# Kernel tuning notes

Measured on AMD Instinct MI355X. Metric: run time of the kernel, lower is better.

Reference implementation:

```python
import jax, jax.numpy as jnp
import numpy as np

D_MODEL = 1024
N_HEADS = 16
HEAD_DIM = D_MODEL // N_HEADS


def setup_inputs() -> dict:
    key = jax.random.key(0)
    k1, k2, k3 = jax.random.split(key, 3)
    x = jax.random.normal(k1, (4, 2048, D_MODEL), dtype=jnp.float32)
    # torch nn.Linear(d_model, 3*d_model, bias=False): weight [3C, C], y = x @ W.T
    w_qkv = jax.random.normal(k2, (3 * D_MODEL, D_MODEL), dtype=jnp.float32) * (1.0 / np.sqrt(D_MODEL))
    w_out = jax.random.normal(k3, (D_MODEL, D_MODEL), dtype=jnp.float32) * (1.0 / np.sqrt(D_MODEL))
    return {"x": x, "w_qkv": w_qkv, "w_out": w_out}


def reference(x, w_qkv, w_out):
    B, T, C = x.shape
    H, Dh = N_HEADS, HEAD_DIM
    scale = 1.0 / np.sqrt(Dh).astype(np.float32)
    qkv = x @ w_qkv.T  # [B, T, 3C]
    q, k, v = jnp.split(qkv, 3, axis=-1)

    def heads(t):  # [B,T,C] -> [B,H,T,Dh]
        return t.reshape(B, T, H, Dh).transpose(0, 2, 1, 3)

    q, k, v = heads(q), heads(k), heads(v)
    attn = jnp.einsum('bhqd,bhkd->bhqk', q, k) * scale  # [B,H,T,T]
    attn = jax.nn.softmax(attn, axis=-1)
    out = jnp.einsum('bhqk,bhkd->bhqd', attn, v)  # [B,H,T,Dh]
    out = out.transpose(0, 2, 1, 3).reshape(B, T, C)
    return out @ w_out.T
```

## Files before the change

kernel.cpp:

```cpp
#include <hip/hip_runtime.h>
#include <hip/hip_bf16.h>

#define DEVINL __device__ __forceinline__

typedef short s16x8 __attribute__((ext_vector_type(8)));
typedef float f32x4 __attribute__((ext_vector_type(4)));

static constexpr int TC = 1024;
static constexpr int NH = 16;
static constexpr int DH = 64;
static constexpr int TT = 2048;
static constexpr int NB = 4;
static constexpr int MROWS = NB * TT;

static constexpr float QSCALE = 0.18033688011112042f;

DEVINL ushort f32_to_bf16u(float f) {
  uint u = __builtin_bit_cast(uint, f);
  u += 0x7fffu + ((u >> 16) & 1u);
  return (ushort)(u >> 16);
}

DEVINL f32x4 mfma32(s16x8 a, s16x8 b, f32x4 c) {
  return __builtin_amdgcn_mfma_f32_16x16x32_bf16(a, b, c, 0, 0, 0);
}

DEVINL void gload_lds16(const void* g, void* l) {
  __builtin_amdgcn_global_load_lds((const __attribute__((address_space(1))) void*)g,
                                   (__attribute__((address_space(3))) void*)l, 16, 0, 0);
}

DEVINL s16x8 ld8(const ushort* p) { return *reinterpret_cast<const s16x8*>(p); }

DEVINL void cvt_range(const float* __restrict__ src, ushort* __restrict__ dst, int n4,
                      int i0, int stride) {
  for (int i = i0; i < n4; i += stride) {
    float4 v = reinterpret_cast<const float4*>(src)[i];
    ushort4 o;
    o.x = f32_to_bf16u(v.x);
    o.y = f32_to_bf16u(v.y);
    o.z = f32_to_bf16u(v.z);
    o.w = f32_to_bf16u(v.w);
    reinterpret_cast<ushort4*>(dst)[i] = o;
  }
}

__global__ void cvt3_kernel(const float* __restrict__ s0, ushort* __restrict__ d0, int n0,
                            const float* __restrict__ s1, ushort* __restrict__ d1, int n1,
                            const float* __restrict__ s2, ushort* __restrict__ d2, int n2) {
  const int i0 = blockIdx.x * blockDim.x + threadIdx.x;
  const int stride = gridDim.x * blockDim.x;
  cvt_range(s0, d0, n0, i0, stride);
  cvt_range(s1, d1, n1, i0, stride);
  cvt_range(s2, d2, n2, i0, stride);
}

template <int MODE>
__global__ __launch_bounds__(256, 2) void gemm_bt(
    const ushort* __restrict__ A, const ushort* __restrict__ Bw, float* __restrict__ Cout,
    ushort* __restrict__ Qo, ushort* __restrict__ Ko, ushort* __restrict__ Vo, int N) {
  __shared__ __align__(16) ushort As[128 * 128];
  __shared__ __align__(16) ushort Bs[128 * 128];
  const int tid = threadIdx.x;
  const int lane = tid & 63;
  const int wid = tid >> 6;
  const int bx = blockIdx.x, by = blockIdx.y;
  const int wrow = (wid >> 1) * 64, wcol = (wid & 1) * 64;

  f32x4 acc[4][4] = {};

  for (int kt = 0; kt < TC; kt += 128) {
#pragma unroll
    for (int j = 0; j < 8; ++j) {
      const int flat = j * 256 + tid;
      const int r = flat >> 4, ch = flat & 15;
      const int sc = ch ^ (r & 15);
      gload_lds16(A + (size_t)(by * 128 + r) * TC + kt + sc * 8, &As[flat * 8]);
      gload_lds16(Bw + (size_t)(bx * 128 + r) * TC + kt + sc * 8, &Bs[flat * 8]);
    }
    __syncthreads();
#pragma unroll
    for (int kk = 0; kk < 4; ++kk) {
      s16x8 af[4], bfr[4];
#pragma unroll
      for (int m = 0; m < 4; ++m) {
        const int r = wrow + m * 16 + (lane & 15);
        const int ch = (kk * 4 + (lane >> 4)) ^ (r & 15);
        af[m] = ld8(&As[r * 128 + ch * 8]);
      }
#pragma unroll
      for (int n = 0; n < 4; ++n) {
        const int r = wcol + n * 16 + (lane & 15);
        const int ch = (kk * 4 + (lane >> 4)) ^ (r & 15);
        bfr[n] = ld8(&Bs[r * 128 + ch * 8]);
      }
#pragma unroll
      for (int m = 0; m < 4; ++m)
#pragma unroll
        for (int n = 0; n < 4; ++n) acc[m][n] = mfma32(af[m], bfr[n], acc[m][n]);
    }
    __syncthreads();
  }

#pragma unroll
  for (int m = 0; m < 4; ++m) {
#pragma unroll
    for (int n = 0; n < 4; ++n) {
      const int ng = bx * 128 + wcol + n * 16 + (lane & 15);
      const int mg0 = by * 128 + wrow + m * 16 + (lane >> 4) * 4;
      if (MODE == 0) {
#pragma unroll
        for (int i = 0; i < 4; ++i) Cout[(size_t)(mg0 + i) * N + ng] = acc[m][n][i];
      } else {
        const int sec = ng >> 10;
        const int w = ng & 1023;
        const int h = w >> 6, d = w & 63;
        const int t0 = mg0 & (TT - 1);
        const int b = mg0 >> 11;
        const int bh = b * NH + h;
        if (sec == 0) {
#pragma unroll
          for (int i = 0; i < 4; ++i)
            Qo[((size_t)bh * TT + t0 + i) * DH + d] = f32_to_bf16u(acc[m][n][i] * QSCALE);
        } else if (sec == 1) {
#pragma unroll
          for (int i = 0; i < 4; ++i)
            Ko[((size_t)bh * TT + t0 + i) * DH + d] = f32_to_bf16u(acc[m][n][i]);
        } else {
          ushort4 o;
          o.x = f32_to_bf16u(acc[m][n][0]);
          o.y = f32_to_bf16u(acc[m][n][1]);
          o.z = f32_to_bf16u(acc[m][n][2]);
          o.w = f32_to_bf16u(acc[m][n][3]);
          *reinterpret_cast<ushort4*>(&Vo[((size_t)bh * DH + d) * TT + t0]) = o;
        }
      }
    }
  }
}

__global__ __launch_bounds__(256, 4) void attn_kernel(const ushort* __restrict__ Q,
                                                      const ushort* __restrict__ K,
                                                      const ushort* __restrict__ V,
                                                      ushort* __restrict__ O) {
  __shared__ __align__(16) ushort Ks[2][64 * 64];
  __shared__ __align__(16) ushort Vs[2][64 * 64];
  const int tid = threadIdx.x;
  const int lane = tid & 63, wid = tid >> 6;
  const int bh = blockIdx.x;
  const int q0 = blockIdx.y * 128 + wid * 32;
  const int qr = lane & 15, lg = lane >> 4;

  const ushort* Qh = Q + (size_t)bh * TT * DH;
  const ushort* Kh = K + (size_t)bh * TT * DH;
  const ushort* Vh = V + (size_t)bh * DH * TT;

  s16x8 qf[2][2];
#pragma unroll
  for (int qt = 0; qt < 2; ++qt)
#pragma unroll
    for (int h = 0; h < 2; ++h)
      qf[qt][h] = ld8(&Qh[(q0 + qt * 16 + qr) * DH + h * 32 + lg * 8]);

  const int pk = 8 * (qr >> 2) + (qr & 3);

  const uint one_bf = 0x3F803F80u;
  const s16x8 ONES = __builtin_bit_cast(s16x8, (uint4){one_bf, one_bf, one_bf, one_bf});

  f32x4 acc[2][4] = {};
  f32x4 acc1[2] = {};

#define SWZ(r) ((r ^ ((r & 8) >> 1)) & 7)

  int koff[2][2][2], voff[2][4];
#pragma unroll
  for (int kh = 0; kh < 2; ++kh) {
#pragma unroll
    for (int jj = 0; jj < 2; ++jj)
#pragma unroll
      for (int h = 0; h < 2; ++h) {
        const int r = kh * 32 + pk + 4 * jj;
        koff[kh][jj][h] = r * 64 + ((h * 4 + lg) ^ SWZ(r)) * 8;
      }
#pragma unroll
    for (int g = 0; g < 4; ++g) {
      const int r = g * 16 + qr;
      voff[kh][g] = r * 64 + ((kh * 4 + lg) ^ SWZ(r)) * 8;
    }
  }

#define STAGE(buf, k0)                                                              \
  {                                                                                 \
    _Pragma("unroll") for (int j = 0; j < 2; ++j) {                                 \
      const int l = tid + 256 * j;                                                  \
      const int row = l >> 3, ch = l & 7;                                           \
      const int sc = ch ^ SWZ(row);                                                 \
      gload_lds16(&Kh[(size_t)((k0) + row) * DH + sc * 8],                          \
                  &Ks[buf][(wid * 64 + 256 * j) * 8]);                              \
      gload_lds16(&Vh[(size_t)row * TT + (k0) + sc * 8],                            \
                  &Vs[buf][(wid * 64 + 256 * j) * 8]);                              \
    }                                                                               \
  }

  STAGE(0, 0);
  __syncthreads();

  for (int t = 0; t < TT / 64; ++t) {
    const int buf = t & 1;
    if (t + 1 < TT / 64) STAGE(buf ^ 1, (t + 1) * 64);
    const ushort* Kb = Ks[buf];
    const ushort* Vb = Vs[buf];

#pragma unroll
    for (int kh = 0; kh < 2; ++kh) {
      s16x8 kf[2][2];
#pragma unroll
      for (int jj = 0; jj < 2; ++jj)
#pragma unroll
        for (int h = 0; h < 2; ++h) kf[jj][h] = ld8(&Kb[koff[kh][jj][h]]);
      s16x8 vf[4];
#pragma unroll
      for (int g = 0; g < 4; ++g) vf[g] = ld8(&Vb[voff[kh][g]]);

#pragma unroll
      for (int qt = 0; qt < 2; ++qt) {
        const f32x4 z = {};
        __builtin_amdgcn_s_setprio(1);
        f32x4 slo = mfma32(kf[0][0], qf[qt][0], z);
        slo = mfma32(kf[0][1], qf[qt][1], slo);
        f32x4 shi = mfma32(kf[1][0], qf[qt][0], z);
        shi = mfma32(kf[1][1], qf[qt][1], shi);
        __builtin_amdgcn_s_setprio(0);

        float p[8];
#pragma unroll
        for (int i = 0; i < 4; ++i) {
          p[i] = __builtin_amdgcn_exp2f(slo[i]);
          p[4 + i] = __builtin_amdgcn_exp2f(shi[i]);
        }

        uint u[4];
#pragma unroll
        for (int e = 0; e < 4; ++e)
          asm("v_cvt_pk_bf16_f32 %0, %1, %2" : "=v"(u[e]) : "v"(p[2 * e]), "v"(p[2 * e + 1]));
        const s16x8 pa = __builtin_bit_cast(s16x8, u);

        __builtin_amdgcn_s_setprio(1);
#pragma unroll
        for (int g = 0; g < 4; ++g) acc[qt][g] = mfma32(pa, vf[g], acc[qt][g]);
        acc1[qt] = mfma32(pa, ONES, acc1[qt]);
        __builtin_amdgcn_s_setprio(0);
      }
    }
    __syncthreads();
  }

  const int b = bh >> 4, h = bh & 15;
#pragma unroll
  for (int qt = 0; qt < 2; ++qt) {
    float inv[4];
#pragma unroll
    for (int i = 0; i < 4; ++i) inv[i] = 1.0f / acc1[qt][i];
#pragma unroll
    for (int g = 0; g < 4; ++g) {
#pragma unroll
      for (int i = 0; i < 4; ++i) {
        const int tq = q0 + qt * 16 + lg * 4 + i;
        const int col = h * DH + g * 16 + qr;
        O[((size_t)b * TT + tq) * TC + col] = f32_to_bf16u(acc[qt][g][i] * inv[i]);
      }
    }
  }
#undef STAGE
#undef SWZ
}

extern "C" void kernel_launch(void* const* d_in, const int* in_sizes, int n_in,
                              void* d_out, int out_size, void* d_ws, size_t ws_size,
                              hipStream_t stream) {
  const float* x = (const float*)d_in[0];
  const float* wqkv = (const float*)d_in[1];
  const float* wout = (const float*)d_in[2];
  float* out = (float*)d_out;
  char* ws = (char*)d_ws;

  ushort* xb    = (ushort*)(ws);
  ushort* wqkvb = (ushort*)(ws + ((size_t)16 << 20));
  ushort* woutb = (ushort*)(ws + ((size_t)22 << 20));
  ushort* qb    = (ushort*)(ws + ((size_t)24 << 20));
  ushort* kb    = (ushort*)(ws + ((size_t)40 << 20));
  ushort* vtb   = (ushort*)(ws + ((size_t)56 << 20));

  cvt3_kernel<<<2048, 256, 0, stream>>>(x, xb, MROWS * TC / 4,
                                        wqkv, wqkvb, 3 * TC * TC / 4,
                                        wout, woutb, TC * TC / 4);

  gemm_bt<1><<<dim3(3 * TC / 128, MROWS / 128), 256, 0, stream>>>(
      xb, wqkvb, nullptr, qb, kb, vtb, 3 * TC);

  attn_kernel<<<dim3(NB * NH, TT / 128), 256, 0, stream>>>(qb, kb, vtb, xb);

  gemm_bt<0><<<dim3(TC / 128, MROWS / 128), 256, 0, stream>>>(
      xb, woutb, out, nullptr, nullptr, nullptr, TC);
}
```

Before: 168.4 us.

## Double-buffer GEMM LDS tiles with 64-wide K stages to overlap loads

```diff
diff --git a/kernel.cpp b/kernel.cpp
--- a/kernel.cpp
+++ b/kernel.cpp
@@ -59,40 +59,51 @@
 __global__ __launch_bounds__(256, 2) void gemm_bt(
     const ushort* __restrict__ A, const ushort* __restrict__ Bw, float* __restrict__ Cout,
     ushort* __restrict__ Qo, ushort* __restrict__ Ko, ushort* __restrict__ Vo, int N) {
-  __shared__ __align__(16) ushort As[128 * 128];
-  __shared__ __align__(16) ushort Bs[128 * 128];
+  __shared__ __align__(16) ushort As[2][128 * 64];
+  __shared__ __align__(16) ushort Bs[2][128 * 64];
   const int tid = threadIdx.x;
   const int lane = tid & 63;
   const int wid = tid >> 6;
   const int bx = blockIdx.x, by = blockIdx.y;
   const int wrow = (wid >> 1) * 64, wcol = (wid & 1) * 64;
+  const int lr = lane >> 3;
+  const int lc = lane & 7;
 
   f32x4 acc[4][4] = {};
 
-  for (int kt = 0; kt < TC; kt += 128) {
-#pragma unroll
-    for (int j = 0; j < 8; ++j) {
-      const int flat = j * 256 + tid;
-      const int r = flat >> 4, ch = flat & 15;
-      const int sc = ch ^ (r & 15);
-      gload_lds16(A + (size_t)(by * 128 + r) * TC + kt + sc * 8, &As[flat * 8]);
-      gload_lds16(Bw + (size_t)(bx * 128 + r) * TC + kt + sc * 8, &Bs[flat * 8]);
-    }
-    __syncthreads();
-#pragma unroll
-    for (int kk = 0; kk < 4; ++kk) {
+#define GSTAGE(buf, kt)                                                         \
+  {                                                                             \
+    _Pragma("unroll") for (int j = 0; j < 4; ++j) {                             \
+      const int seg = wid * 4 + j;                                              \
+      const int r = seg * 8 + lr;                                               \
+      const int csrc = lc ^ (r & 7);                                            \
+      gload_lds16(A + (size_t)(by * 128 + r) * TC + (kt) + csrc * 8,            \
+                  &As[buf][seg * 512]);                                         \
+      gload_lds16(Bw + (size_t)(bx * 128 + r) * TC + (kt) + csrc * 8,           \
+                  &Bs[buf][seg * 512]);                                         \
+    }                                                                           \
+  }
+
+  GSTAGE(0, 0);
+  __syncthreads();
+
+  for (int t = 0; t < TC / 64; ++t) {
+    const int buf = t & 1;
+    if (t + 1 < TC / 64) GSTAGE(buf ^ 1, (t + 1) * 64);
+#pragma unroll
+    for (int kk = 0; kk < 2; ++kk) {
       s16x8 af[4], bfr[4];
 #pragma unroll
       for (int m = 0; m < 4; ++m) {
         const int r = wrow + m * 16 + (lane & 15);
-        const int ch = (kk * 4 + (lane >> 4)) ^ (r & 15);
-        af[m] = ld8(&As[r * 128 + ch * 8]);
+        const int ch = (kk * 4 + (lane >> 4)) ^ (r & 7);
+        af[m] = ld8(&As[buf][r * 64 + ch * 8]);
       }
 #pragma unroll
       for (int n = 0; n < 4; ++n) {
         const int r = wcol + n * 16 + (lane & 15);
-        const int ch = (kk * 4 + (lane >> 4)) ^ (r & 15);
-        bfr[n] = ld8(&Bs[r * 128 + ch * 8]);
+        const int ch = (kk * 4 + (lane >> 4)) ^ (r & 7);
+        bfr[n] = ld8(&Bs[buf][r * 64 + ch * 8]);
       }
 #pragma unroll
       for (int m = 0; m < 4; ++m)
@@ -101,6 +112,7 @@
     }
     __syncthreads();
   }
+#undef GSTAGE
 
 #pragma unroll
   for (int m = 0; m < 4; ++m) {
```

Measured after the change: 175.3 us. +4.1%, slower.
